# Performance work log

Hardware: AMD Instinct MI355X
Metric: run time of the kernel (lower is better)

The kernel has to match this reference:

```python
import jax, jax.numpy as jnp
import numpy as np

B, C, T, D = 32, 64, 30000, 64

def setup_inputs() -> dict:
    key = jax.random.key(0)
    ks = jax.random.split(key, 7)
    s = 1.0  # Linear(1,d): fan_in=1, torch init bound=1
    return {
        "x": jax.random.normal(ks[0], (B, C, T), dtype=jnp.float32),
        "Wq": jax.random.normal(ks[1], (D, 1), dtype=jnp.float32) * s,
        "bq": jax.random.normal(ks[2], (D,), dtype=jnp.float32) * s,
        "Wk": jax.random.normal(ks[3], (D, 1), dtype=jnp.float32) * s,
        "bk": jax.random.normal(ks[4], (D,), dtype=jnp.float32) * s,
        "Wv": jax.random.normal(ks[5], (D, 1), dtype=jnp.float32) * s,
        "bv": jax.random.normal(ks[6], (D,), dtype=jnp.float32) * s,
        "alpha": jnp.float32(0.5),
    }

def reference(x, Wq, bq, Wk, bk, Wv, bv, alpha):
    # x: (B, C, T)
    scale = jnp.asarray(D, x.dtype) ** 0.5
    desc = jnp.mean(x, axis=2, keepdims=True)          # (B, C, 1)
    q = desc * Wq[:, 0] + bq                            # (B, C, D)
    k = desc * Wk[:, 0] + bk                            # (B, C, D)
    # v = desc * Wv[:, 0] + bv  # computed in original but unused downstream
    attn_logits = jnp.einsum('bcd,bed->bce', q, k) / scale  # (B, C, C)
    attn = jax.nn.softmax(attn_logits, axis=-1)             # dropout = identity (eval)
    mixed = jnp.einsum('bce,bet->bct', attn, x)             # (B, C, T)
    return x + alpha * mixed
```

## Files before the change

kernel.cpp:

```cpp
#include <hip/hip_runtime.h>

#define B_DIM 32
#define C_DIM 64
#define D_DIM 64
#define T_DIM 30000
#define T4    7500
#define JTILE 128
#define TILES 235
#define NWG   (TILES * B_DIM)

typedef short bf16x8 __attribute__((ext_vector_type(8)));
typedef float f32x16 __attribute__((ext_vector_type(16)));
typedef float f32x4  __attribute__((ext_vector_type(4)));

__device__ __forceinline__ unsigned short f32_to_bf16_rne(float f) {
    unsigned int u = __builtin_bit_cast(unsigned int, f);
    return (unsigned short)((u + 0x7fffu + ((u >> 16) & 1u)) >> 16);
}

__global__ __launch_bounds__(256) void mean_kernel(const float* __restrict__ x,
                                                   float* __restrict__ desc) {
    int r = blockIdx.x;
    const float4* xr = (const float4*)(x + (size_t)r * T_DIM);
    float4 s = {0.f, 0.f, 0.f, 0.f};
    for (int i = threadIdx.x; i < T4; i += 256) {
        float4 v = xr[i];
        s.x += v.x; s.y += v.y; s.z += v.z; s.w += v.w;
    }
    float p = (s.x + s.y) + (s.z + s.w);
    #pragma unroll
    for (int off = 32; off > 0; off >>= 1) p += __shfl_down(p, off, 64);
    __shared__ float wsum[4];
    int wave = threadIdx.x >> 6;
    int lane = threadIdx.x & 63;
    if (lane == 0) wsum[wave] = p;
    __syncthreads();
    if (threadIdx.x == 0) {
        float tot = (wsum[0] + wsum[1]) + (wsum[2] + wsum[3]);
        desc[r] = tot * (1.0f / (float)T_DIM);
    }
}

__global__ __launch_bounds__(64) void attn_kernel(const float* __restrict__ desc,
                                                  const float* __restrict__ Wq,
                                                  const float* __restrict__ bq,
                                                  const float* __restrict__ Wk,
                                                  const float* __restrict__ bk,
                                                  const float* __restrict__ alphap,
                                                  unsigned short* __restrict__ attnb) {
    int b = blockIdx.x;
    int c = threadIdx.x;
    __shared__ float sd[C_DIM];
    sd[c] = desc[b * C_DIM + c];
    __syncthreads();

    float dA = 0.f, dBq = 0.f, dBk = 0.f, dCc = 0.f;
    #pragma unroll
    for (int d = 0; d < D_DIM; ++d) {
        float wq = Wq[d], wk = Wk[d], vq = bq[d], vk = bk[d];
        dA  += wq * wk;
        dBq += wq * vk;
        dBk += vq * wk;
        dCc += vq * vk;
    }

    float dc = sd[c];
    float l[C_DIM];
    float lmax = -1e30f;
    #pragma unroll
    for (int e = 0; e < C_DIM; ++e) {
        float de = sd[e];
        float v = (dA * dc * de + dBq * dc + dBk * de + dCc) * 0.125f;
        l[e] = v;
        lmax = fmaxf(lmax, v);
    }
    float sum = 0.f;
    #pragma unroll
    for (int e = 0; e < C_DIM; ++e) {
        float ev = __expf(l[e] - lmax);
        l[e] = ev;
        sum += ev;
    }
    float inv = alphap[0] / sum;
    unsigned short* arow = attnb + ((size_t)b * C_DIM + c) * C_DIM;
    #pragma unroll
    for (int e = 0; e < C_DIM; ++e) {
        float v = l[e] * inv + (e == c ? 1.0f : 0.0f);
        arow[e] = f32_to_bf16_rne(v);
    }
}

__global__ __launch_bounds__(256) void mix_mfma(const float* __restrict__ x,
                                                const unsigned short* __restrict__ attnb,
                                                float* __restrict__ out) {
    __shared__ float lx[C_DIM][JTILE];

    int flat = blockIdx.x;
    int swz  = (flat & 7) * (NWG / 8) + (flat >> 3);
    int b    = swz / TILES;
    int tile = swz % TILES;

    int t   = threadIdx.x;
    int w   = t >> 6;
    int l31 = t & 31;
    int lhi = (t >> 5) & 1;

    const unsigned short* ab = attnb + (size_t)b * C_DIM * C_DIM;
    bf16x8 afrag[2][4];
    #pragma unroll
    for (int m = 0; m < 2; ++m)
        #pragma unroll
        for (int g = 0; g < 4; ++g)
            afrag[m][g] = *(const bf16x8*)(ab + (32 * m + l31) * C_DIM + 16 * g + 8 * lhi);

    const float* xb = x + (size_t)b * C_DIM * T_DIM;
    int cf4  = t & 31;
    int jf4  = tile * 32 + cf4;
    int jf4c = (jf4 < T4) ? jf4 : (T4 - 1);
    #pragma unroll
    for (int p = 0; p < 8; ++p) {
        int e = p * 8 + (t >> 5);
        f32x4 v = *(const f32x4*)(xb + (size_t)e * T_DIM + (size_t)jf4c * 4);
        *(f32x4*)&lx[e][cf4 * 4] = v;
    }
    __syncthreads();

    int jc = w * 32 + l31;
    f32x16 acc0 = {}, acc1 = {};
    #pragma unroll
    for (int g = 0; g < 4; ++g) {
        int e0 = 16 * g + 8 * lhi;
        bf16x8 bfrag;
        #pragma unroll
        for (int i = 0; i < 8; ++i)
            bfrag[i] = (short)f32_to_bf16_rne(lx[e0 + i][jc]);
        acc0 = __builtin_amdgcn_mfma_f32_32x32x16_bf16(afrag[0][g], bfrag, acc0, 0, 0, 0);
        acc1 = __builtin_amdgcn_mfma_f32_32x32x16_bf16(afrag[1][g], bfrag, acc1, 0, 0, 0);
    }
    __syncthreads();

    #pragma unroll
    for (int r = 0; r < 16; ++r) {
        int crow = (r & 3) + 8 * (r >> 2) + 4 * lhi;
        lx[crow][jc]      = acc0[r];
        lx[crow + 32][jc] = acc1[r];
    }
    __syncthreads();

    if (jf4 < T4) {
        float* ob = out + (size_t)b * C_DIM * T_DIM;
        #pragma unroll
        for (int p = 0; p < 8; ++p) {
            int e = p * 8 + (t >> 5);
            f32x4 v = *(const f32x4*)&lx[e][cf4 * 4];
            __builtin_nontemporal_store(v, (f32x4*)(ob + (size_t)e * T_DIM + (size_t)jf4 * 4));
        }
    }
}

extern "C" void kernel_launch(void* const* d_in, const int* in_sizes, int n_in,
                              void* d_out, int out_size, void* d_ws, size_t ws_size,
                              hipStream_t stream) {
    const float* x     = (const float*)d_in[0];
    const float* Wq    = (const float*)d_in[1];
    const float* bq    = (const float*)d_in[2];
    const float* Wk    = (const float*)d_in[3];
    const float* bk    = (const float*)d_in[4];
    const float* alpha = (const float*)d_in[7];
    float* out = (float*)d_out;

    float* desc = (float*)d_ws;
    unsigned short* attnb = (unsigned short*)(desc + B_DIM * C_DIM);

    mean_kernel<<<B_DIM * C_DIM, 256, 0, stream>>>(x, desc);
    attn_kernel<<<B_DIM, 64, 0, stream>>>(desc, Wq, bq, Wk, bk, alpha, attnb);
    mix_mfma<<<NWG, 256, 0, stream>>>(x, attnb, out);
}
```

Before: 121.0 us.

## Make mix kernel persistent with double-buffered bf16 LDS staging and register prefetch

Replaces the one-tile-per-block mix kernel with a persistent grid of 1024 blocks. Each block walks a contiguous range of (batch, tile) work items, assigned per XCD. The next tile's x data is prefetched into registers and converted to bf16 into a second LDS buffer while the current tile runs through MFMA, and the attention fragments are reloaded only when the batch changes. The goal is to overlap global loads with compute and cut LDS footprint and launch/tail overhead. The cost is more barriers and output written in two half passes through the reused buffer, and the result still depends on the memory-bound traffic.

```diff
diff --git a/kernel.cpp b/kernel.cpp
--- a/kernel.cpp
+++ b/kernel.cpp
@@ -5,13 +5,17 @@
 #define D_DIM 64
 #define T_DIM 30000
 #define T4    7500
-#define JTILE 128
+#define JT    128
 #define TILES 235
-#define NWG   (TILES * B_DIM)
+#define WORK  (B_DIM * TILES)
+#define WPX   (WORK / 8)
+#define GRID  1024
+#define BPX   (GRID / 8)
 
 typedef short bf16x8 __attribute__((ext_vector_type(8)));
 typedef float f32x16 __attribute__((ext_vector_type(16)));
 typedef float f32x4  __attribute__((ext_vector_type(4)));
+typedef unsigned short u16x8 __attribute__((ext_vector_type(8)));
 
 __device__ __forceinline__ unsigned short f32_to_bf16_rne(float f) {
     unsigned int u = __builtin_bit_cast(unsigned int, f);
@@ -90,71 +94,115 @@
     }
 }
 
-__global__ __launch_bounds__(256) void mix_mfma(const float* __restrict__ x,
-                                                const unsigned short* __restrict__ attnb,
-                                                float* __restrict__ out) {
-    __shared__ float lx[C_DIM][JTILE];
-
-    int flat = blockIdx.x;
-    int swz  = (flat & 7) * (NWG / 8) + (flat >> 3);
-    int b    = swz / TILES;
-    int tile = swz % TILES;
-
-    int t   = threadIdx.x;
-    int w   = t >> 6;
-    int l31 = t & 31;
-    int lhi = (t >> 5) & 1;
-
-    const unsigned short* ab = attnb + (size_t)b * C_DIM * C_DIM;
+__global__ __launch_bounds__(256, 4) void mix2(const float* __restrict__ x,
+                                               const unsigned short* __restrict__ attnb,
+                                               float* __restrict__ out) {
+    __shared__ unsigned short xbuf[2][C_DIM][JT];
+
+    int g   = blockIdx.x;
+    int xcd = g & 7;
+    int idx = g >> 3;
+    int start = xcd * WPX + ((idx * WPX) >> 7);
+    int end   = xcd * WPX + (((idx + 1) * WPX) >> 7);
+
+    int t    = threadIdx.x;
+    int w    = t >> 6;
+    int l31  = t & 31;
+    int lhi  = (t >> 5) & 1;
+    int jc   = w * 32 + l31;
+    int srow = t >> 4;
+    int c16  = t & 15;
+
+    f32x4 R[4][2];
+
+    auto issueLoads = [&](int item) {
+        int b    = item / TILES;
+        int tile = item - b * TILES;
+        const float* xb = x + (size_t)b * C_DIM * T_DIM;
+        int j0 = tile * JT + c16 * 8;
+        if (j0 > T_DIM - 8) j0 = T_DIM - 8;
+        #pragma unroll
+        for (int p = 0; p < 4; ++p) {
+            const float* src = xb + (size_t)(srow + 16 * p) * T_DIM + j0;
+            R[p][0] = *(const f32x4*)(src);
+            R[p][1] = *(const f32x4*)(src + 4);
+        }
+    };
+    auto writeStage = [&](int buf) {
+        #pragma unroll
+        for (int p = 0; p < 4; ++p) {
+            u16x8 v;
+            #pragma unroll
+            for (int q = 0; q < 4; ++q) v[q]     = f32_to_bf16_rne(R[p][0][q]);
+            #pragma unroll
+            for (int q = 0; q < 4; ++q) v[4 + q] = f32_to_bf16_rne(R[p][1][q]);
+            *(u16x8*)&xbuf[buf][srow + 16 * p][c16 * 8] = v;
+        }
+    };
+
     bf16x8 afrag[2][4];
-    #pragma unroll
-    for (int m = 0; m < 2; ++m)
-        #pragma unroll
-        for (int g = 0; g < 4; ++g)
-            afrag[m][g] = *(const bf16x8*)(ab + (32 * m + l31) * C_DIM + 16 * g + 8 * lhi);
-
-    const float* xb = x + (size_t)b * C_DIM * T_DIM;
-    int cf4  = t & 31;
-    int jf4  = tile * 32 + cf4;
-    int jf4c = (jf4 < T4) ? jf4 : (T4 - 1);
-    #pragma unroll
-    for (int p = 0; p < 8; ++p) {
-        int e = p * 8 + (t >> 5);
-        f32x4 v = *(const f32x4*)(xb + (size_t)e * T_DIM + (size_t)jf4c * 4);
-        *(f32x4*)&lx[e][cf4 * 4] = v;
-    }
+    int bprev = -1;
+    int cur = 0;
+
+    issueLoads(start);
+    writeStage(0);
+    issueLoads(start + 1 < end ? start + 1 : start);
     __syncthreads();
 
-    int jc = w * 32 + l31;
-    f32x16 acc0 = {}, acc1 = {};
-    #pragma unroll
-    for (int g = 0; g < 4; ++g) {
-        int e0 = 16 * g + 8 * lhi;
-        bf16x8 bfrag;
-        #pragma unroll
-        for (int i = 0; i < 8; ++i)
-            bfrag[i] = (short)f32_to_bf16_rne(lx[e0 + i][jc]);
-        acc0 = __builtin_amdgcn_mfma_f32_32x32x16_bf16(afrag[0][g], bfrag, acc0, 0, 0, 0);
-        acc1 = __builtin_amdgcn_mfma_f32_32x32x16_bf16(afrag[1][g], bfrag, acc1, 0, 0, 0);
-    }
-    __syncthreads();
-
-    #pragma unroll
-    for (int r = 0; r < 16; ++r) {
-        int crow = (r & 3) + 8 * (r >> 2) + 4 * lhi;
-        lx[crow][jc]      = acc0[r];
-        lx[crow + 32][jc] = acc1[r];
-    }
-    __syncthreads();
-
-    if (jf4 < T4) {
+    for (int item = start; item < end; ++item) {
+        int b    = item / TILES;
+        int tile = item - b * TILES;
+
+        if (b != bprev) {
+            const unsigned short* ab = attnb + (size_t)b * C_DIM * C_DIM;
+            #pragma unroll
+            for (int m = 0; m < 2; ++m)
+                #pragma unroll
+                for (int gg = 0; gg < 4; ++gg)
+                    afrag[m][gg] = *(const bf16x8*)(ab + (32 * m + l31) * C_DIM + 16 * gg + 8 * lhi);
+            bprev = b;
+        }
+
+        f32x16 acc0 = {}, acc1 = {};
+        #pragma unroll
+        for (int gg = 0; gg < 4; ++gg) {
+            int e0 = 16 * gg + 8 * lhi;
+            bf16x8 bfrag;
+            #pragma unroll
+            for (int i = 0; i < 8; ++i)
+                bfrag[i] = (short)xbuf[cur][e0 + i][jc];
+            acc0 = __builtin_amdgcn_mfma_f32_32x32x16_bf16(afrag[0][gg], bfrag, acc0, 0, 0, 0);
+            acc1 = __builtin_amdgcn_mfma_f32_32x32x16_bf16(afrag[1][gg], bfrag, acc1, 0, 0, 0);
+        }
+
+        if (item + 1 < end) {
+            writeStage(cur ^ 1);
+            issueLoads(item + 2 < end ? item + 2 : end - 1);
+        }
+        __syncthreads();
+
+        float (*o)[JT] = (float (*)[JT]) &xbuf[cur][0][0];
         float* ob = out + (size_t)b * C_DIM * T_DIM;
         #pragma unroll
-        for (int p = 0; p < 8; ++p) {
-            int e = p * 8 + (t >> 5);
-            f32x4 v = *(const f32x4*)&lx[e][cf4 * 4];
-            __builtin_nontemporal_store(v, (f32x4*)(ob + (size_t)e * T_DIM + (size_t)jf4 * 4));
-        }
+        for (int h = 0; h < 2; ++h) {
+            #pragma unroll
+            for (int r = 0; r < 16; ++r) {
+                int crow = (r & 3) + 8 * (r >> 2) + 4 * lhi;
+                o[crow][jc] = h ? acc1[r] : acc0[r];
+            }
+            __syncthreads();
+            #pragma unroll
+            for (int p = 0; p < 4; ++p) {
+                int row  = (t >> 5) + 8 * p;
+                f32x4 v  = *(const f32x4*)&o[row][(t & 31) * 4];
+                int gcol = tile * JT + (t & 31) * 4;
+                if (gcol + 3 < T_DIM)
+                    __builtin_nontemporal_store(
+                        v, (f32x4*)(ob + (size_t)(h * 32 + row) * T_DIM + gcol));
+            }
+            __syncthreads();
+        }
+        cur ^= 1;
     }
 }
 
@@ -174,5 +222,5 @@
 
     mean_kernel<<<B_DIM * C_DIM, 256, 0, stream>>>(x, desc);
     attn_kernel<<<B_DIM, 64, 0, stream>>>(desc, Wq, bq, Wk, bk, alpha, attnb);
-    mix_mfma<<<NWG, 256, 0, stream>>>(x, attnb, out);
-}
+    mix2<<<GRID, 256, 0, stream>>>(x, attnb, out);
+}
```

Result: no change. 122.0 us (+0.8%).

## Fuse mean and attention kernels via last-block atomic counter; reverse tile order

Applied to the files above, without the earlier changes.

Merges the mean reduction and the softmax-attention computation into one kernel. The last block to finish, detected with an atomic counter after a threadfence, computes all 2048 attention rows with 256 threads. This removes one kernel launch. It adds a memset and a serial tail in a single workgroup that recomputes the exponentials. Separately, the mix kernel walks tiles in reverse order, presumably so it starts on the x data most recently brought into cache by the mean pass.

```diff
diff --git a/kernel.cpp b/kernel.cpp
--- a/kernel.cpp
+++ b/kernel.cpp
@@ -8,6 +8,7 @@
 #define JTILE 128
 #define TILES 235
 #define NWG   (TILES * B_DIM)
+#define ROWS  (B_DIM * C_DIM)
 
 typedef short bf16x8 __attribute__((ext_vector_type(8)));
 typedef float f32x16 __attribute__((ext_vector_type(16)));
@@ -18,8 +19,15 @@
     return (unsigned short)((u + 0x7fffu + ((u >> 16) & 1u)) >> 16);
 }
 
-__global__ __launch_bounds__(256) void mean_kernel(const float* __restrict__ x,
-                                                   float* __restrict__ desc) {
+__global__ __launch_bounds__(256) void mean_attn_kernel(const float* __restrict__ x,
+                                                        const float* __restrict__ Wq,
+                                                        const float* __restrict__ bq,
+                                                        const float* __restrict__ Wk,
+                                                        const float* __restrict__ bk,
+                                                        const float* __restrict__ alphap,
+                                                        float* __restrict__ desc,
+                                                        unsigned short* __restrict__ attnb,
+                                                        int* __restrict__ counter) {
     int r = blockIdx.x;
     const float4* xr = (const float4*)(x + (size_t)r * T_DIM);
     float4 s = {0.f, 0.f, 0.f, 0.f};
@@ -35,27 +43,19 @@
     int lane = threadIdx.x & 63;
     if (lane == 0) wsum[wave] = p;
     __syncthreads();
+
+    __shared__ int win;
     if (threadIdx.x == 0) {
         float tot = (wsum[0] + wsum[1]) + (wsum[2] + wsum[3]);
         desc[r] = tot * (1.0f / (float)T_DIM);
+        __threadfence();
+        win = (atomicAdd(counter, 1) == ROWS - 1);
     }
-}
-
-__global__ __launch_bounds__(64) void attn_kernel(const float* __restrict__ desc,
-                                                  const float* __restrict__ Wq,
-                                                  const float* __restrict__ bq,
-                                                  const float* __restrict__ Wk,
-                                                  const float* __restrict__ bk,
-                                                  const float* __restrict__ alphap,
-                                                  unsigned short* __restrict__ attnb) {
-    int b = blockIdx.x;
-    int c = threadIdx.x;
-    __shared__ float sd[C_DIM];
-    sd[c] = desc[b * C_DIM + c];
     __syncthreads();
+    if (!win) return;
+    __threadfence();
 
     float dA = 0.f, dBq = 0.f, dBk = 0.f, dCc = 0.f;
-    #pragma unroll
     for (int d = 0; d < D_DIM; ++d) {
         float wq = Wq[d], wk = Wk[d], vq = bq[d], vk = bk[d];
         dA  += wq * wk;
@@ -63,30 +63,29 @@
         dBk += vq * wk;
         dCc += vq * vk;
     }
+    float alpha = alphap[0];
 
-    float dc = sd[c];
-    float l[C_DIM];
-    float lmax = -1e30f;
     #pragma unroll
-    for (int e = 0; e < C_DIM; ++e) {
-        float de = sd[e];
-        float v = (dA * dc * de + dBq * dc + dBk * de + dCc) * 0.125f;
-        l[e] = v;
-        lmax = fmaxf(lmax, v);
-    }
-    float sum = 0.f;
-    #pragma unroll
-    for (int e = 0; e < C_DIM; ++e) {
-        float ev = __expf(l[e] - lmax);
-        l[e] = ev;
-        sum += ev;
-    }
-    float inv = alphap[0] / sum;
-    unsigned short* arow = attnb + ((size_t)b * C_DIM + c) * C_DIM;
-    #pragma unroll
-    for (int e = 0; e < C_DIM; ++e) {
-        float v = l[e] * inv + (e == c ? 1.0f : 0.0f);
-        arow[e] = f32_to_bf16_rne(v);
+    for (int it = 0; it < 8; ++it) {
+        int idx = threadIdx.x + 256 * it;
+        int b = idx >> 6, c = idx & 63;
+        const float* db = desc + b * C_DIM;
+        float dc = db[c];
+        float base = dBq * dc + dCc;
+        float coef = dA * dc + dBk;
+        float lmax = -1e30f;
+        for (int e = 0; e < C_DIM; ++e)
+            lmax = fmaxf(lmax, (coef * db[e] + base) * 0.125f);
+        float sum = 0.f;
+        for (int e = 0; e < C_DIM; ++e)
+            sum += __expf((coef * db[e] + base) * 0.125f - lmax);
+        float inv = alpha / sum;
+        unsigned short* arow = attnb + (size_t)idx * C_DIM;
+        for (int e = 0; e < C_DIM; ++e) {
+            float v = __expf((coef * db[e] + base) * 0.125f - lmax) * inv
+                      + (e == c ? 1.0f : 0.0f);
+            arow[e] = f32_to_bf16_rne(v);
+        }
     }
 }
 
@@ -98,7 +97,7 @@
     int flat = blockIdx.x;
     int swz  = (flat & 7) * (NWG / 8) + (flat >> 3);
     int b    = swz / TILES;
-    int tile = swz % TILES;
+    int tile = (TILES - 1) - (swz % TILES);
 
     int t   = threadIdx.x;
     int w   = t >> 6;
@@ -170,9 +169,11 @@
     float* out = (float*)d_out;
 
     float* desc = (float*)d_ws;
-    unsigned short* attnb = (unsigned short*)(desc + B_DIM * C_DIM);
+    unsigned short* attnb = (unsigned short*)(desc + ROWS);
+    int* counter = (int*)(attnb + (size_t)B_DIM * C_DIM * C_DIM);
 
-    mean_kernel<<<B_DIM * C_DIM, 256, 0, stream>>>(x, desc);
-    attn_kernel<<<B_DIM, 64, 0, stream>>>(desc, Wq, bq, Wk, bk, alpha, attnb);
+    hipMemsetAsync(counter, 0, sizeof(int), stream);
+    mean_attn_kernel<<<ROWS, 256, 0, stream>>>(x, Wq, bq, Wk, bk, alpha,
+                                               desc, attnb, counter);
     mix_mfma<<<NWG, 256, 0, stream>>>(x, attnb, out);
 }
```

Result: slower. 236.1 us (+95.1%).

## Stage bf16 copy of x during mean pass and feed mixing kernel from it

Applied to the files above, without the earlier changes.

The mean kernel now also converts x to bf16 and writes it to a workspace buffer. The mixing kernel reads that half-size bf16 copy instead of re-reading fp32 x and converting it in the MFMA loop, and it stores results in two halves through LDS. The aim is to halve the read bytes in the mix pass and let the freshly written smaller copy stay in the last-level cache. The cost is an extra write of about 123 MB in the first pass. A fallback keeps the old path when the workspace is too small.

```diff
diff --git a/kernel.cpp b/kernel.cpp
--- a/kernel.cpp
+++ b/kernel.cpp
@@ -5,18 +5,131 @@
 #define D_DIM 64
 #define T_DIM 30000
 #define T4    7500
+#define T8    3750
 #define JTILE 128
 #define TILES 235
 #define NWG   (TILES * B_DIM)
+#define ROWS  (B_DIM * C_DIM)
 
 typedef short bf16x8 __attribute__((ext_vector_type(8)));
 typedef float f32x16 __attribute__((ext_vector_type(16)));
 typedef float f32x4  __attribute__((ext_vector_type(4)));
+typedef unsigned short u16x8 __attribute__((ext_vector_type(8)));
 
 __device__ __forceinline__ unsigned short f32_to_bf16_rne(float f) {
     unsigned int u = __builtin_bit_cast(unsigned int, f);
     return (unsigned short)((u + 0x7fffu + ((u >> 16) & 1u)) >> 16);
 }
+
+
+__global__ __launch_bounds__(256) void mean_bf16_kernel(const float* __restrict__ x,
+                                                        float* __restrict__ desc,
+                                                        unsigned short* __restrict__ xb) {
+    int r = blockIdx.x;
+    const f32x4* xr = (const f32x4*)(x + (size_t)r * T_DIM);
+    u16x8* br = (u16x8*)(xb + (size_t)r * T_DIM);
+    f32x4 s = {0.f, 0.f, 0.f, 0.f};
+    for (int i = threadIdx.x; i < T8; i += 256) {
+        f32x4 a = __builtin_nontemporal_load(xr + 2 * i);
+        f32x4 c = __builtin_nontemporal_load(xr + 2 * i + 1);
+        s += a; s += c;
+        u16x8 v;
+        #pragma unroll
+        for (int q = 0; q < 4; ++q) v[q]     = f32_to_bf16_rne(a[q]);
+        #pragma unroll
+        for (int q = 0; q < 4; ++q) v[4 + q] = f32_to_bf16_rne(c[q]);
+        br[i] = v;
+    }
+    float p = (s.x + s.y) + (s.z + s.w);
+    #pragma unroll
+    for (int off = 32; off > 0; off >>= 1) p += __shfl_down(p, off, 64);
+    __shared__ float wsum[4];
+    int wave = threadIdx.x >> 6;
+    int lane = threadIdx.x & 63;
+    if (lane == 0) wsum[wave] = p;
+    __syncthreads();
+    if (threadIdx.x == 0) {
+        float tot = (wsum[0] + wsum[1]) + (wsum[2] + wsum[3]);
+        desc[r] = tot * (1.0f / (float)T_DIM);
+    }
+}
+
+__global__ __launch_bounds__(256) void mix_bf16(const unsigned short* __restrict__ xb,
+                                                const unsigned short* __restrict__ attnb,
+                                                float* __restrict__ out) {
+    __shared__ unsigned short lh[C_DIM][JTILE];
+
+    int flat = blockIdx.x;
+    int swz  = (flat & 7) * (NWG / 8) + (flat >> 3);
+    int b    = swz / TILES;
+    int tile = swz % TILES;
+
+    int t   = threadIdx.x;
+    int w   = t >> 6;
+    int l31 = t & 31;
+    int lhi = (t >> 5) & 1;
+
+    const unsigned short* ab = attnb + (size_t)b * C_DIM * C_DIM;
+    bf16x8 afrag[2][4];
+    #pragma unroll
+    for (int m = 0; m < 2; ++m)
+        #pragma unroll
+        for (int g = 0; g < 4; ++g)
+            afrag[m][g] = *(const bf16x8*)(ab + (32 * m + l31) * C_DIM + 16 * g + 8 * lhi);
+
+    const unsigned short* xrow = xb + (size_t)b * C_DIM * T_DIM;
+    #pragma unroll
+    for (int p = 0; p < 4; ++p) {
+        int chunk = t + 256 * p;
+        int e  = chunk >> 4;
+        int c8 = chunk & 15;
+        int j0 = tile * JTILE + c8 * 8;
+        if (j0 > T_DIM - 8) j0 = T_DIM - 8;
+        u16x8 v = *(const u16x8*)(xrow + (size_t)e * T_DIM + j0);
+        *(u16x8*)&lh[e][c8 * 8] = v;
+    }
+    __syncthreads();
+
+    int jc = w * 32 + l31;
+    f32x16 acc0 = {}, acc1 = {};
+    #pragma unroll
+    for (int g = 0; g < 4; ++g) {
+        int e0 = 16 * g + 8 * lhi;
+        bf16x8 bfrag;
+        #pragma unroll
+        for (int i = 0; i < 8; ++i)
+            bfrag[i] = (short)lh[e0 + i][jc];
+        acc0 = __builtin_amdgcn_mfma_f32_32x32x16_bf16(afrag[0][g], bfrag, acc0, 0, 0, 0);
+        acc1 = __builtin_amdgcn_mfma_f32_32x32x16_bf16(afrag[1][g], bfrag, acc1, 0, 0, 0);
+    }
+    __syncthreads();
+
+    float (*o)[JTILE] = (float (*)[JTILE]) &lh[0][0];
+    float* ob = out + (size_t)b * C_DIM * T_DIM;
+    #pragma unroll
+    for (int h = 0; h < 2; ++h) {
+        #pragma unroll
+        for (int r = 0; r < 16; ++r) {
+            int crow = (r & 3) + 8 * (r >> 2) + 4 * lhi;
+            o[crow][jc] = h ? acc1[r] : acc0[r];
+        }
+        __syncthreads();
+        #pragma unroll
+        for (int p = 0; p < 4; ++p) {
+            int chunk = t + 256 * p;
+            int row = chunk >> 5;
+            int c4  = chunk & 31;
+            int gcol = tile * JTILE + c4 * 4;
+            if (gcol + 3 < T_DIM) {
+                f32x4 v = *(const f32x4*)&o[row][c4 * 4];
+                __builtin_nontemporal_store(
+                    v, (f32x4*)(ob + (size_t)(h * 32 + row) * T_DIM + gcol));
+            }
+        }
+        __syncthreads();
+    }
+}
+
 
 __global__ __launch_bounds__(256) void mean_kernel(const float* __restrict__ x,
                                                    float* __restrict__ desc) {
@@ -40,6 +153,75 @@
         desc[r] = tot * (1.0f / (float)T_DIM);
     }
 }
+
+__global__ __launch_bounds__(256) void mix_mfma(const float* __restrict__ x,
+                                                const unsigned short* __restrict__ attnb,
+                                                float* __restrict__ out) {
+    __shared__ float lx[C_DIM][JTILE];
+
+    int flat = blockIdx.x;
+    int swz  = (flat & 7) * (NWG / 8) + (flat >> 3);
+    int b    = swz / TILES;
+    int tile = swz % TILES;
+
+    int t   = threadIdx.x;
+    int w   = t >> 6;
+    int l31 = t & 31;
+    int lhi = (t >> 5) & 1;
+
+    const unsigned short* ab = attnb + (size_t)b * C_DIM * C_DIM;
+    bf16x8 afrag[2][4];
+    #pragma unroll
+    for (int m = 0; m < 2; ++m)
+        #pragma unroll
+        for (int g = 0; g < 4; ++g)
+            afrag[m][g] = *(const bf16x8*)(ab + (32 * m + l31) * C_DIM + 16 * g + 8 * lhi);
+
+    const float* xbp = x + (size_t)b * C_DIM * T_DIM;
+    int cf4  = t & 31;
+    int jf4  = tile * 32 + cf4;
+    int jf4c = (jf4 < T4) ? jf4 : (T4 - 1);
+    #pragma unroll
+    for (int p = 0; p < 8; ++p) {
+        int e = p * 8 + (t >> 5);
+        f32x4 v = *(const f32x4*)(xbp + (size_t)e * T_DIM + (size_t)jf4c * 4);
+        *(f32x4*)&lx[e][cf4 * 4] = v;
+    }
+    __syncthreads();
+
+    int jc = w * 32 + l31;
+    f32x16 acc0 = {}, acc1 = {};
+    #pragma unroll
+    for (int g = 0; g < 4; ++g) {
+        int e0 = 16 * g + 8 * lhi;
+        bf16x8 bfrag;
+        #pragma unroll
+        for (int i = 0; i < 8; ++i)
+            bfrag[i] = (short)f32_to_bf16_rne(lx[e0 + i][jc]);
+        acc0 = __builtin_amdgcn_mfma_f32_32x32x16_bf16(afrag[0][g], bfrag, acc0, 0, 0, 0);
+        acc1 = __builtin_amdgcn_mfma_f32_32x32x16_bf16(afrag[1][g], bfrag, acc1, 0, 0, 0);
+    }
+    __syncthreads();
+
+    #pragma unroll
+    for (int r = 0; r < 16; ++r) {
+        int crow = (r & 3) + 8 * (r >> 2) + 4 * lhi;
+        lx[crow][jc]      = acc0[r];
+        lx[crow + 32][jc] = acc1[r];
+    }
+    __syncthreads();
+
+    if (jf4 < T4) {
+        float* ob = out + (size_t)b * C_DIM * T_DIM;
+        #pragma unroll
+        for (int p = 0; p < 8; ++p) {
+            int e = p * 8 + (t >> 5);
+            f32x4 v = *(const f32x4*)&lx[e][cf4 * 4];
+            __builtin_nontemporal_store(v, (f32x4*)(ob + (size_t)e * T_DIM + (size_t)jf4 * 4));
+        }
+    }
+}
+
 
 __global__ __launch_bounds__(64) void attn_kernel(const float* __restrict__ desc,
                                                   const float* __restrict__ Wq,
@@ -90,74 +272,6 @@
     }
 }
 
-__global__ __launch_bounds__(256) void mix_mfma(const float* __restrict__ x,
-                                                const unsigned short* __restrict__ attnb,
-                                                float* __restrict__ out) {
-    __shared__ float lx[C_DIM][JTILE];
-
-    int flat = blockIdx.x;
-    int swz  = (flat & 7) * (NWG / 8) + (flat >> 3);
-    int b    = swz / TILES;
-    int tile = swz % TILES;
-
-    int t   = threadIdx.x;
-    int w   = t >> 6;
-    int l31 = t & 31;
-    int lhi = (t >> 5) & 1;
-
-    const unsigned short* ab = attnb + (size_t)b * C_DIM * C_DIM;
-    bf16x8 afrag[2][4];
-    #pragma unroll
-    for (int m = 0; m < 2; ++m)
-        #pragma unroll
-        for (int g = 0; g < 4; ++g)
-            afrag[m][g] = *(const bf16x8*)(ab + (32 * m + l31) * C_DIM + 16 * g + 8 * lhi);
-
-    const float* xb = x + (size_t)b * C_DIM * T_DIM;
-    int cf4  = t & 31;
-    int jf4  = tile * 32 + cf4;
-    int jf4c = (jf4 < T4) ? jf4 : (T4 - 1);
-    #pragma unroll
-    for (int p = 0; p < 8; ++p) {
-        int e = p * 8 + (t >> 5);
-        f32x4 v = *(const f32x4*)(xb + (size_t)e * T_DIM + (size_t)jf4c * 4);
-        *(f32x4*)&lx[e][cf4 * 4] = v;
-    }
-    __syncthreads();
-
-    int jc = w * 32 + l31;
-    f32x16 acc0 = {}, acc1 = {};
-    #pragma unroll
-    for (int g = 0; g < 4; ++g) {
-        int e0 = 16 * g + 8 * lhi;
-        bf16x8 bfrag;
-        #pragma unroll
-        for (int i = 0; i < 8; ++i)
-            bfrag[i] = (short)f32_to_bf16_rne(lx[e0 + i][jc]);
-        acc0 = __builtin_amdgcn_mfma_f32_32x32x16_bf16(afrag[0][g], bfrag, acc0, 0, 0, 0);
-        acc1 = __builtin_amdgcn_mfma_f32_32x32x16_bf16(afrag[1][g], bfrag, acc1, 0, 0, 0);
-    }
-    __syncthreads();
-
-    #pragma unroll
-    for (int r = 0; r < 16; ++r) {
-        int crow = (r & 3) + 8 * (r >> 2) + 4 * lhi;
-        lx[crow][jc]      = acc0[r];
-        lx[crow + 32][jc] = acc1[r];
-    }
-    __syncthreads();
-
-    if (jf4 < T4) {
-        float* ob = out + (size_t)b * C_DIM * T_DIM;
-        #pragma unroll
-        for (int p = 0; p < 8; ++p) {
-            int e = p * 8 + (t >> 5);
-            f32x4 v = *(const f32x4*)&lx[e][cf4 * 4];
-            __builtin_nontemporal_store(v, (f32x4*)(ob + (size_t)e * T_DIM + (size_t)jf4 * 4));
-        }
-    }
-}
-
 extern "C" void kernel_launch(void* const* d_in, const int* in_sizes, int n_in,
                               void* d_out, int out_size, void* d_ws, size_t ws_size,
                               hipStream_t stream) {
@@ -170,9 +284,19 @@
     float* out = (float*)d_out;
 
     float* desc = (float*)d_ws;
-    unsigned short* attnb = (unsigned short*)(desc + B_DIM * C_DIM);
-
-    mean_kernel<<<B_DIM * C_DIM, 256, 0, stream>>>(x, desc);
-    attn_kernel<<<B_DIM, 64, 0, stream>>>(desc, Wq, bq, Wk, bk, alpha, attnb);
-    mix_mfma<<<NWG, 256, 0, stream>>>(x, attnb, out);
-}
+    unsigned short* attnb = (unsigned short*)(desc + ROWS);
+    unsigned short* xb = attnb + (size_t)B_DIM * C_DIM * C_DIM;
+
+    size_t need = (size_t)ROWS * 4 + (size_t)B_DIM * C_DIM * C_DIM * 2
+                + (size_t)B_DIM * C_DIM * T_DIM * 2;
+
+    if (ws_size >= need) {
+        mean_bf16_kernel<<<ROWS, 256, 0, stream>>>(x, desc, xb);
+        attn_kernel<<<B_DIM, 64, 0, stream>>>(desc, Wq, bq, Wk, bk, alpha, attnb);
+        mix_bf16<<<NWG, 256, 0, stream>>>(xb, attnb, out);
+    } else {
+        mean_kernel<<<ROWS, 256, 0, stream>>>(x, desc);
+        attn_kernel<<<B_DIM, 64, 0, stream>>>(desc, Wq, bq, Wk, bk, alpha, attnb);
+        mix_mfma<<<NWG, 256, 0, stream>>>(x, attnb, out);
+    }
+}
```

Measured after the change: 138.4 us. 14.4% more time.
